# Optimization experiments

Hardware: AMD Instinct MI355X
Metric: run time of the kernel (lower is better)

The kernel has to match this reference:

```python
import jax, jax.numpy as jnp
import numpy as np

N_PHY = 12
NMUL = 4
WARM_UP = 365
NEARZERO = 1e-5
LENF = 15

# parameter_bounds order: BETA, FC, K0, K1, K2, LP, PERC, UZL, TT, CFMAX, CFR, CWH
PHY_LB = jnp.array([1.0, 50.0, 0.05, 0.01, 0.001, 0.2, 0.0, 0.0, -2.5, 0.5, 0.0, 0.0], dtype=jnp.float32)
PHY_UB = jnp.array([6.0, 1000.0, 0.9, 0.5, 0.2, 1.0, 10.0, 100.0, 2.5, 10.0, 0.1, 0.2], dtype=jnp.float32)
ROUTE_A_LB, ROUTE_A_UB = 0.0, 2.9
ROUTE_B_LB, ROUTE_B_UB = 0.0, 6.5


def _hbv_scan(p, t, pet, states, phy):
    """Run HBV step recurrence over time. p/t/pet: [T,G]; states: 5-tuple of [G,M]."""
    beta, fc, k0, k1, k2, lp, perc, uzl, tt, cfmax, cfr, cwh = phy  # each [G,M]

    def step(carry, xt):
        snowpack, meltwater, sm, suz, slz = carry
        Pt, Tt, PETt = xt
        Pt, Tt, PETt = Pt[:, None], Tt[:, None], PETt[:, None]  # [G,1] bcast vs [G,M]
        is_rain = (Tt >= tt).astype(sm.dtype)
        rain = Pt * is_rain
        snow = Pt * (1.0 - is_rain)
        snowpack = snowpack + snow
        melt = jnp.minimum(jnp.maximum(cfmax * (Tt - tt), 0.0), snowpack)
        meltwater = meltwater + melt
        snowpack = snowpack - melt
        refreeze = jnp.minimum(jnp.maximum(cfr * cfmax * (tt - Tt), 0.0), meltwater)
        snowpack = snowpack + refreeze
        meltwater = meltwater - refreeze
        tosoil = jnp.maximum(meltwater - cwh * snowpack, 0.0)
        meltwater = meltwater - tosoil
        soil_wetness = jnp.clip((sm / fc) ** beta, 0.0, 1.0)
        recharge = (rain + tosoil) * soil_wetness
        sm = sm + rain + tosoil - recharge
        excess = jnp.maximum(sm - fc, 0.0)
        sm = sm - excess
        evapfactor = jnp.clip(sm / (lp * fc), 0.0, 1.0)
        etact = jnp.minimum(sm, PETt * evapfactor)
        sm = jnp.maximum(sm - etact, NEARZERO)
        suz = suz + recharge + excess
        prc = jnp.minimum(suz, perc)
        suz = suz - prc
        q0 = k0 * jnp.maximum(suz - uzl, 0.0)
        suz = suz - q0
        q1 = k1 * suz
        suz = suz - q1
        slz = slz + prc
        q2 = k2 * slz
        slz = slz - q2
        return (snowpack, meltwater, sm, suz, slz), q0 + q1 + q2

    states, qs = jax.lax.scan(step, states, (p, t, pet))
    return qs, states  # qs: [T,G,M]


def _forward(x_phy, parameters):
    T, G, _ = x_phy.shape
    p, t, pet = x_phy[..., 0], x_phy[..., 1], x_phy[..., 2]
    # unpack physical params from last param timestep, map [0,1] -> bounds
    raw = parameters[-1, :, : N_PHY * NMUL].reshape(G, N_PHY, NMUL)
    phy_all = PHY_LB[None, :, None] + raw * (PHY_UB - PHY_LB)[None, :, None]
    phy = tuple(phy_all[:, i, :] for i in range(N_PHY))  # (beta, fc, k0, k1, k2, lp, perc, uzl, tt, cfmax, cfr, cwh)
    route = parameters[-1, :, N_PHY * NMUL :]
    a = ROUTE_A_LB + route[:, 0] * (ROUTE_A_UB - ROUTE_A_LB)
    b = ROUTE_B_LB + route[:, 1] * (ROUTE_B_UB - ROUTE_B_LB)

    s0 = jnp.full((G, NMUL), 0.001, dtype=x_phy.dtype)
    states = (s0, s0, s0, s0, s0)

    # warm-up under stop_gradient (matches torch.no_grad in original)
    phy_ng = jax.tree_util.tree_map(jax.lax.stop_gradient, phy)
    q_warm, states = _hbv_scan(
        jax.lax.stop_gradient(p[:WARM_UP]),
        jax.lax.stop_gradient(t[:WARM_UP]),
        jax.lax.stop_gradient(pet[:WARM_UP]),
        states, phy_ng)
    states = jax.tree_util.tree_map(jax.lax.stop_gradient, states)
    q_warm = jax.lax.stop_gradient(q_warm)

    q_pred, _ = _hbv_scan(p[WARM_UP:], t[WARM_UP:], pet[WARM_UP:], states, phy)
    qs = jnp.concatenate([q_warm, q_pred], axis=0).mean(-1)  # [T,G]

    # gamma unit hydrograph weights, [LENF, G]
    tg = (jnp.arange(LENF, dtype=qs.dtype) + 0.5)[:, None]
    aa = jax.nn.relu(a)[None, :] + 0.1
    th = jax.nn.relu(b)[None, :] + 0.5
    w = (tg ** (aa - 1.0)) * jnp.exp(-tg / th) / (jnp.exp(jax.scipy.special.gammaln(aa)) * th ** aa)
    w = w / w.sum(0)

    # causal depthwise (per-basin) convolution along time
    conv = jax.vmap(lambda q, u: jnp.convolve(q, u)[:T])(qs.T, w.T)  # [G,T]
    streamflow = conv.T[:, :, None]  # [T,G,1]
    return streamflow[WARM_UP:]


def setup_inputs() -> dict:
    key = jax.random.key(0)
    k1, k2, k3, k4 = jax.random.split(key, 4)
    T, G = 2000, 4000
    prcp = jax.random.uniform(k1, (T, G), dtype=jnp.float32) * 10.0   # mm/day
    tmean = jax.random.normal(k2, (T, G), dtype=jnp.float32) * 8.0    # degC
    pet = jax.random.uniform(k3, (T, G), dtype=jnp.float32) * 5.0     # mm/day
    x_phy = jnp.stack([prcp, tmean, pet], axis=-1)
    parameters = jax.random.uniform(k4, (1, G, N_PHY * NMUL + 2), dtype=jnp.float32)
    return {"x_phy": x_phy, "parameters": parameters}


def reference(x_phy, parameters):
    return _forward(x_phy, parameters)
```

## Files before the change

kernel.cpp:

```cpp
#include <hip/hip_runtime.h>

#define TT    2000
#define NG    4000
#define WARM  365
#define LENF  15
#define NPHY  12
#define BLK   60
#define NBLK  34
#define SLOTW 64
#define SLOT  (BLK * SLOTW)
#define ROWF  (3 * NG)

typedef const float __attribute__((address_space(1)))* gptr_t;
typedef float __attribute__((address_space(3)))* lptr_t;
typedef __attribute__((ext_vector_type(4))) float f32x4;

__device__ __forceinline__ float quad_sum(float x) {
    int a = __builtin_amdgcn_update_dpp(0, __float_as_int(x), 0xB1, 0xF, 0xF, true);
    float s = x + __int_as_float(a);
    int b = __builtin_amdgcn_update_dpp(0, __float_as_int(s), 0x4E, 0xF, 0xF, true);
    return s + __int_as_float(b);
}

#define WG_BARRIER() asm volatile("s_waitcnt lgkmcnt(0)\n\ts_barrier" ::: "memory")

__global__ __launch_bounds__(256, 1) void hbv_pipe_kernel(
    const float* __restrict__ xphy,
    const float* __restrict__ prm,
    float* __restrict__ out)
{
    __shared__ float s_stage[2 * SLOT];
    __shared__ f32x4 s_rtev[2 * (BLK / 2) * 64];
    __shared__ f32x4 s_rex [2 * (BLK / 4) * 64];
    __shared__ f32x4 s_q   [2 * (BLK / 4) * 64];

    const int lane = threadIdx.x & 63;
    const int wid  = threadIdx.x >> 6;
    const int g0   = blockIdx.x * 16;
    const int cell = lane >> 2;
    const int g    = g0 + cell;
    const int m    = lane & 3;

    const float* pg = prm + (size_t)g * (NPHY * 4 + 2);

    const float lb[NPHY] = {1.0f, 50.0f, 0.05f, 0.01f, 0.001f, 0.2f, 0.0f, 0.0f, -2.5f, 0.5f, 0.0f, 0.0f};
    const float ub[NPHY] = {6.0f, 1000.0f, 0.9f, 0.5f, 0.2f, 1.0f, 10.0f, 100.0f, 2.5f, 10.0f, 0.1f, 0.2f};
    float ph[NPHY];
    #pragma unroll
    for (int i = 0; i < NPHY; ++i)
        ph[i] = lb[i] + pg[i * 4 + m] * (ub[i] - lb[i]);

    const float beta = ph[0], fc = ph[1], k0 = ph[2], k1 = ph[3], k2 = ph[4],
                lp = ph[5], perc = ph[6], uzl = ph[7], ttp = ph[8],
                cfmax = ph[9], cfr = ph[10], cwh = ph[11];
    const float rlpfc  = 1.0f / (lp * fc);
    const float cfrcf  = cfr * cfmax;
    const float blfc   = beta * __builtin_amdgcn_logf(1.0f / fc);
    const float onemk1 = 1.0f - k1;
    const float onemk2 = 1.0f - k2;

    const float aa  = fmaxf(pg[48] * 2.9f, 0.0f) + 0.1f;
    const float th  = fmaxf(pg[49] * 6.5f, 0.0f) + 0.5f;
    const float rth = 1.0f / th;
    const float LOG2E = 1.4426950408889634f;
    float w[LENF];
    float wsum = 0.0f;
    #pragma unroll
    for (int k = 0; k < LENF; ++k) {
        const float tg = (float)k + 0.5f;
        const float e = (aa - 1.0f) * __builtin_log2f(tg) - tg * rth * LOG2E;
        w[k] = __builtin_amdgcn_exp2f(e);
        wsum += w[k];
    }
    const float rw = 0.25f / wsum;
    #pragma unroll
    for (int k = 0; k < LENF; ++k) w[k] *= rw;

    float snowpack = 0.001f, meltwater = 0.001f;
    float sm = 0.001f;
    float suz = 0.001f, slz = 0.001f;
    float qh[BLK + LENF - 1];
    #pragma unroll
    for (int d = 0; d < BLK + LENF - 1; ++d) qh[d] = 0.0f;

    const int loffd = (lane < 48 ? lane : 47);

    auto stage_blk = [&](int b) {
        const int tb = b * BLK + wid * 15;
        float* ldst = &s_stage[(b & 1) * SLOT + (wid * 15) * SLOTW];
        #pragma unroll
        for (int c = 0; c < 15; ++c) {
            int t = tb + c; t = (t < TT) ? t : (TT - 1);
            const float* src = xphy + (size_t)t * ROWF + g0 * 3 + loffd;
            __builtin_amdgcn_global_load_lds((gptr_t)src, (lptr_t)(ldst + c * SLOTW), 4, 0, 0);
        }
    };

    stage_blk(0);
    asm volatile("s_waitcnt vmcnt(0)" ::: "memory");
    WG_BARRIER();

    for (int i = 0; i <= NBLK + 2; ++i) {
        if (i + 1 < NBLK) stage_blk(i + 1);

        if (wid == 0) {
            if (i < NBLK) {
                const float* sb = &s_stage[(i & 1) * SLOT + cell * 3];
                f32x4* rtw = &s_rtev[(i & 1) * ((BLK / 2) * 64) + lane];
                float rtE = 0.0f, evE = 0.0f;
                #pragma unroll
                for (int j = 0; j < BLK; ++j) {
                    const float Pt = sb[j * SLOTW];
                    const float Tm = sb[j * SLOTW + 1];
                    const float ev = sb[j * SLOTW + 2];
                    const float dT      = Tm - ttp;
                    const float rain    = (Tm >= ttp) ? Pt : 0.0f;
                    const float snw     = Pt - rain;
                    const float meltcap = cfmax * fmaxf(dT, 0.0f);
                    const float refcap  = cfrcf * fmaxf(-dT, 0.0f);
                    snowpack += snw;
                    const float melt = fminf(meltcap, snowpack);
                    meltwater += melt;
                    snowpack  -= melt;
                    const float refreeze = fminf(refcap, meltwater);
                    meltwater -= refreeze;
                    snowpack  += refreeze;
                    const float tosoil = fmaxf(fmaf(-cwh, snowpack, meltwater), 0.0f);
                    meltwater -= tosoil;
                    const float rt = rain + tosoil;
                    if ((j & 1) == 0) { rtE = rt; evE = ev; }
                    else {
                        f32x4 q; q[0] = rtE; q[1] = evE; q[2] = rt; q[3] = ev;
                        rtw[(j >> 1) * 64] = q;
                    }
                }
            }
            asm volatile("s_waitcnt vmcnt(0)" ::: "memory");
        } else if (wid == 1) {
            const int b = i - 1;
            if (b >= 0 && b < NBLK) {
                const f32x4* rtr = &s_rtev[(b & 1) * ((BLK / 2) * 64) + lane];
                f32x4* rexw = &s_rex[(b & 1) * ((BLK / 4) * 64) + lane];
                f32x4 rp; rp[0] = 0.0f; rp[1] = 0.0f; rp[2] = 0.0f; rp[3] = 0.0f;
                float x0 = 0.0f, x1 = 0.0f, x2 = 0.0f;
                #pragma unroll
                for (int j = 0; j < BLK; ++j) {
                    if ((j & 1) == 0) rp = rtr[(j >> 1) * 64];
                    const float rt = ((j & 1) == 0) ? rp[0] : rp[2];
                    const float ev = ((j & 1) == 0) ? rp[1] : rp[3];
                    const float sw  = __builtin_amdgcn_exp2f(fmaf(beta, __builtin_amdgcn_logf(sm), blfc));
                    const float sp  = sm + rt;
                    const float sm1 = fmaf(-rt, sw, sp);
                    const float sm2 = fminf(sm1, fc);
                    const float uf  = fmaxf(fmaf(-ev, rlpfc, 1.0f), 0.0f);
                    sm = fmaxf(fmaxf(sm2 * uf, sm2 - ev), 1e-5f);
                    const float rex = fmaf(rt, sw, sm1 - sm2);
                    if ((j & 3) == 0)      x0 = rex;
                    else if ((j & 3) == 1) x1 = rex;
                    else if ((j & 3) == 2) x2 = rex;
                    else {
                        f32x4 q; q[0] = x0; q[1] = x1; q[2] = x2; q[3] = rex;
                        rexw[(j >> 2) * 64] = q;
                    }
                }
            }
            asm volatile("s_waitcnt vmcnt(0)" ::: "memory");
        } else if (wid == 2) {
            const int b = i - 2;
            if (b >= 0 && b < NBLK) {
                const f32x4* rexr = &s_rex[(b & 1) * ((BLK / 4) * 64) + lane];
                f32x4* qw = &s_q[(b & 1) * ((BLK / 4) * 64) + lane];
                f32x4 rp; rp[0] = 0.0f; rp[1] = 0.0f; rp[2] = 0.0f; rp[3] = 0.0f;
                float q0v = 0.0f, q1v = 0.0f, q2v = 0.0f;
                #pragma unroll
                for (int j = 0; j < BLK; ++j) {
                    if ((j & 3) == 0) rp = rexr[(j >> 2) * 64];
                    const float rex = ((j & 3) == 0) ? rp[0] : ((j & 3) == 1) ? rp[1]
                                     : ((j & 3) == 2) ? rp[2] : rp[3];
                    const float suz1 = suz + rex;
                    const float prc  = fminf(suz1, perc);
                    const float suzA = suz1 - prc;
                    const float tq   = fmaxf(suzA - uzl, 0.0f);
                    const float q0   = k0 * tq;
                    const float suzB = fmaf(-k0, tq, suzA);
                    const float q1   = k1 * suzB;
                    suz = suzB * onemk1;
                    const float sl1  = slz + prc;
                    const float q2   = k2 * sl1;
                    slz = sl1 * onemk2;
                    const float q = quad_sum(q0 + q1 + q2);
                    if ((j & 3) == 0)      q0v = q;
                    else if ((j & 3) == 1) q1v = q;
                    else if ((j & 3) == 2) q2v = q;
                    else {
                        f32x4 qq; qq[0] = q0v; qq[1] = q1v; qq[2] = q2v; qq[3] = q;
                        qw[(j >> 2) * 64] = qq;
                    }
                }
            }
            asm volatile("s_waitcnt vmcnt(0)" ::: "memory");
        } else {
            const int b = i - 3;
            if (b >= 0 && b < NBLK) {
                const int t0 = b * BLK;
                const f32x4* qr = &s_q[(b & 1) * ((BLK / 4) * 64) + lane];
                #pragma unroll
                for (int p = 0; p < BLK / 4; ++p) {
                    const f32x4 qq = qr[p * 64];
                    qh[LENF - 1 + 4 * p]     = qq[0];
                    qh[LENF - 1 + 4 * p + 1] = qq[1];
                    qh[LENF - 1 + 4 * p + 2] = qq[2];
                    qh[LENF - 1 + 4 * p + 3] = qq[3];
                }
                float ov[BLK / 4];
                #pragma unroll
                for (int k = 0; k < BLK / 4; ++k) ov[k] = 0.0f;
                #pragma unroll
                for (int j = 0; j < BLK; ++j) {
                    float o = w[0] * qh[LENF - 1 + j];
                    #pragma unroll
                    for (int k = 1; k < LENF; ++k)
                        o = fmaf(w[k], qh[LENF - 1 + j - k], o);
                    const bool sel = ((j & 3) == m);
                    ov[j >> 2] = sel ? o : ov[j >> 2];
                }
                #pragma unroll
                for (int d = 0; d < LENF - 1; ++d) qh[d] = qh[d + BLK];
                #pragma unroll
                for (int k = 0; k < BLK / 4; ++k) {
                    const int j = k * 4 + m;
                    const int t = t0 + j;
                    if (t >= WARM && t < TT)
                        out[(size_t)(t - WARM) * NG + g] = ov[k];
                }
            }
            asm volatile("s_waitcnt vmcnt(0)" ::: "memory");
        }

        WG_BARRIER();
    }
}

extern "C" void kernel_launch(void* const* d_in, const int* in_sizes, int n_in,
                              void* d_out, int out_size, void* d_ws, size_t ws_size,
                              hipStream_t stream) {
    const float* xphy = (const float*)d_in[0];
    const float* prm  = (const float*)d_in[1];
    float* out = (float*)d_out;

    hbv_pipe_kernel<<<NG / 16, 256, 0, stream>>>(xphy, prm, out);
}
```

Measured before the change: 146.7 us.

## Stage inputs with 16-byte loads from the conv wave only; pair LDS handoffs

Input staging moves from all four waves issuing 4-byte global_load_lds per timestep to only the last (convolution) wave issuing 16-byte loads covering four timesteps per instruction. The staged layout changes to a 4-float stride per cell, so the snow wave reads each timestep with one vector LDS load. The per-wave vmcnt waits in the recurrence waves are dropped, taking memory latency off the serial critical path. Inter-stage LDS buffers switch from float4 to float2 packing, which flushes results every two steps instead of four. The risk is that 16-byte loads reading 3-float records into 4-float slots pick up a neighbouring value, and that staging concentrated in one wave may not finish before the barrier.

```diff
diff --git a/kernel.cpp b/kernel.cpp
--- a/kernel.cpp
+++ b/kernel.cpp
@@ -13,6 +13,7 @@
 
 typedef const float __attribute__((address_space(1)))* gptr_t;
 typedef float __attribute__((address_space(3)))* lptr_t;
+typedef __attribute__((ext_vector_type(2))) float f32x2;
 typedef __attribute__((ext_vector_type(4))) float f32x4;
 
 __device__ __forceinline__ float quad_sum(float x) {
@@ -31,8 +32,8 @@
 {
     __shared__ float s_stage[2 * SLOT];
     __shared__ f32x4 s_rtev[2 * (BLK / 2) * 64];
-    __shared__ f32x4 s_rex [2 * (BLK / 4) * 64];
-    __shared__ f32x4 s_q   [2 * (BLK / 4) * 64];
+    __shared__ f32x2 s_rex [2 * (BLK / 2) * 64];
+    __shared__ f32x2 s_q   [2 * (BLK / 2) * 64];
 
     const int lane = threadIdx.x & 63;
     const int wid  = threadIdx.x >> 6;
@@ -83,36 +84,37 @@
     #pragma unroll
     for (int d = 0; d < BLK + LENF - 1; ++d) qh[d] = 0.0f;
 
-    const int loffd = (lane < 48 ? lane : 47);
+    const int s4 = lane >> 4;
+    const int c4 = lane & 15;
 
     auto stage_blk = [&](int b) {
-        const int tb = b * BLK + wid * 15;
-        float* ldst = &s_stage[(b & 1) * SLOT + (wid * 15) * SLOTW];
+        float* lbase = &s_stage[(b & 1) * SLOT];
         #pragma unroll
-        for (int c = 0; c < 15; ++c) {
-            int t = tb + c; t = (t < TT) ? t : (TT - 1);
-            const float* src = xphy + (size_t)t * ROWF + g0 * 3 + loffd;
-            __builtin_amdgcn_global_load_lds((gptr_t)src, (lptr_t)(ldst + c * SLOTW), 4, 0, 0);
+        for (int ld = 0; ld < 15; ++ld) {
+            int t = b * BLK + ld * 4 + s4;
+            t = (t < TT) ? t : (TT - 1);
+            const float* src = xphy + (size_t)t * ROWF + (g0 + c4) * 3;
+            __builtin_amdgcn_global_load_lds((gptr_t)src,
+                (lptr_t)(lbase + ld * 4 * SLOTW), 16, 0, 0);
         }
     };
 
-    stage_blk(0);
-    asm volatile("s_waitcnt vmcnt(0)" ::: "memory");
+    if (wid == 3) {
+        stage_blk(0);
+        asm volatile("s_waitcnt vmcnt(0)" ::: "memory");
+    }
     WG_BARRIER();
 
     for (int i = 0; i <= NBLK + 2; ++i) {
-        if (i + 1 < NBLK) stage_blk(i + 1);
-
         if (wid == 0) {
             if (i < NBLK) {
-                const float* sb = &s_stage[(i & 1) * SLOT + cell * 3];
+                const f32x4* sb = (const f32x4*)&s_stage[(i & 1) * SLOT + cell * 4];
                 f32x4* rtw = &s_rtev[(i & 1) * ((BLK / 2) * 64) + lane];
                 float rtE = 0.0f, evE = 0.0f;
                 #pragma unroll
                 for (int j = 0; j < BLK; ++j) {
-                    const float Pt = sb[j * SLOTW];
-                    const float Tm = sb[j * SLOTW + 1];
-                    const float ev = sb[j * SLOTW + 2];
+                    const f32x4 x = sb[j * 16];
+                    const float Pt = x[0], Tm = x[1], ev = x[2];
                     const float dT      = Tm - ttp;
                     const float rain    = (Tm >= ttp) ? Pt : 0.0f;
                     const float snw     = Pt - rain;
@@ -135,14 +137,13 @@
                     }
                 }
             }
-            asm volatile("s_waitcnt vmcnt(0)" ::: "memory");
         } else if (wid == 1) {
             const int b = i - 1;
             if (b >= 0 && b < NBLK) {
                 const f32x4* rtr = &s_rtev[(b & 1) * ((BLK / 2) * 64) + lane];
-                f32x4* rexw = &s_rex[(b & 1) * ((BLK / 4) * 64) + lane];
+                f32x2* rexw = &s_rex[(b & 1) * ((BLK / 2) * 64) + lane];
                 f32x4 rp; rp[0] = 0.0f; rp[1] = 0.0f; rp[2] = 0.0f; rp[3] = 0.0f;
-                float x0 = 0.0f, x1 = 0.0f, x2 = 0.0f;
+                float rexE = 0.0f;
                 #pragma unroll
                 for (int j = 0; j < BLK; ++j) {
                     if ((j & 1) == 0) rp = rtr[(j >> 1) * 64];
@@ -155,28 +156,21 @@
                     const float uf  = fmaxf(fmaf(-ev, rlpfc, 1.0f), 0.0f);
                     sm = fmaxf(fmaxf(sm2 * uf, sm2 - ev), 1e-5f);
                     const float rex = fmaf(rt, sw, sm1 - sm2);
-                    if ((j & 3) == 0)      x0 = rex;
-                    else if ((j & 3) == 1) x1 = rex;
-                    else if ((j & 3) == 2) x2 = rex;
-                    else {
-                        f32x4 q; q[0] = x0; q[1] = x1; q[2] = x2; q[3] = rex;
-                        rexw[(j >> 2) * 64] = q;
-                    }
-                }
-            }
-            asm volatile("s_waitcnt vmcnt(0)" ::: "memory");
+                    if ((j & 1) == 0) rexE = rex;
+                    else { f32x2 pr; pr[0] = rexE; pr[1] = rex; rexw[(j >> 1) * 64] = pr; }
+                }
+            }
         } else if (wid == 2) {
             const int b = i - 2;
             if (b >= 0 && b < NBLK) {
-                const f32x4* rexr = &s_rex[(b & 1) * ((BLK / 4) * 64) + lane];
-                f32x4* qw = &s_q[(b & 1) * ((BLK / 4) * 64) + lane];
-                f32x4 rp; rp[0] = 0.0f; rp[1] = 0.0f; rp[2] = 0.0f; rp[3] = 0.0f;
-                float q0v = 0.0f, q1v = 0.0f, q2v = 0.0f;
-                #pragma unroll
-                for (int j = 0; j < BLK; ++j) {
-                    if ((j & 3) == 0) rp = rexr[(j >> 2) * 64];
-                    const float rex = ((j & 3) == 0) ? rp[0] : ((j & 3) == 1) ? rp[1]
-                                     : ((j & 3) == 2) ? rp[2] : rp[3];
+                const f32x2* rexr = &s_rex[(b & 1) * ((BLK / 2) * 64) + lane];
+                f32x2* qw = &s_q[(b & 1) * ((BLK / 2) * 64) + lane];
+                f32x2 rp; rp[0] = 0.0f; rp[1] = 0.0f;
+                float qE = 0.0f;
+                #pragma unroll
+                for (int j = 0; j < BLK; ++j) {
+                    if ((j & 1) == 0) rp = rexr[(j >> 1) * 64];
+                    const float rex = ((j & 1) == 0) ? rp[0] : rp[1];
                     const float suz1 = suz + rex;
                     const float prc  = fminf(suz1, perc);
                     const float suzA = suz1 - prc;
@@ -189,28 +183,21 @@
                     const float q2   = k2 * sl1;
                     slz = sl1 * onemk2;
                     const float q = quad_sum(q0 + q1 + q2);
-                    if ((j & 3) == 0)      q0v = q;
-                    else if ((j & 3) == 1) q1v = q;
-                    else if ((j & 3) == 2) q2v = q;
-                    else {
-                        f32x4 qq; qq[0] = q0v; qq[1] = q1v; qq[2] = q2v; qq[3] = q;
-                        qw[(j >> 2) * 64] = qq;
-                    }
-                }
-            }
-            asm volatile("s_waitcnt vmcnt(0)" ::: "memory");
+                    if ((j & 1) == 0) qE = q;
+                    else { f32x2 pr; pr[0] = qE; pr[1] = q; qw[(j >> 1) * 64] = pr; }
+                }
+            }
         } else {
+            if (i + 1 < NBLK) stage_blk(i + 1);
             const int b = i - 3;
             if (b >= 0 && b < NBLK) {
                 const int t0 = b * BLK;
-                const f32x4* qr = &s_q[(b & 1) * ((BLK / 4) * 64) + lane];
-                #pragma unroll
-                for (int p = 0; p < BLK / 4; ++p) {
-                    const f32x4 qq = qr[p * 64];
-                    qh[LENF - 1 + 4 * p]     = qq[0];
-                    qh[LENF - 1 + 4 * p + 1] = qq[1];
-                    qh[LENF - 1 + 4 * p + 2] = qq[2];
-                    qh[LENF - 1 + 4 * p + 3] = qq[3];
+                const f32x2* qr = &s_q[(b & 1) * ((BLK / 2) * 64) + lane];
+                #pragma unroll
+                for (int p = 0; p < BLK / 2; ++p) {
+                    const f32x2 qq = qr[p * 64];
+                    qh[LENF - 1 + 2 * p]     = qq[0];
+                    qh[LENF - 1 + 2 * p + 1] = qq[1];
                 }
                 float ov[BLK / 4];
                 #pragma unroll
```

After: 134.8 us. -8.1%, faster.
